# Kernel tuning notes

Measured on AMD Instinct MI355X. Metric: run time of the kernel, lower is better.

## Reference

```python
import jax, jax.numpy as jnp
import numpy as np

# Each of the 16 differentiable binary logic ops op_k(a,b) is a polynomial
# c0 + ca*a + cb*b + cab*(a*b). Rows follow the standard difflogic op table
# (op 3 = 'a' pass-through, matching the residual init in the source).
_OP2POLY = np.array([
    [0, 0, 0, 0],    # 0: False
    [0, 0, 0, 1],    # 1: a AND b
    [0, 1, 0, -1],   # 2: a AND NOT b
    [0, 1, 0, 0],    # 3: a
    [0, 0, 1, -1],   # 4: NOT a AND b
    [0, 0, 1, 0],    # 5: b
    [0, 1, 1, -2],   # 6: XOR
    [0, 1, 1, -1],   # 7: OR
    [1, -1, -1, 1],  # 8: NOR
    [1, -1, -1, 2],  # 9: XNOR
    [1, 0, -1, 0],   # 10: NOT b
    [1, 0, -1, 1],   # 11: a OR NOT b
    [1, -1, 0, 0],   # 12: NOT a
    [1, -1, 0, 1],   # 13: NOT a OR b
    [1, 0, 0, -1],   # 14: NAND
    [1, 0, 0, 0],    # 15: True
], dtype=np.float32)

KERNEL_SIZE, STRIDE, PADDING, GROUPS, TREE_DEPTH, TAU = 3, 1, 1, 1, 4, 1.0


def setup_inputs() -> dict:
    key = jax.random.key(0)
    k0, k1, k2, k3, k4 = jax.random.split(key, 5)
    B, Cin, H, W = 16, 64, 64, 64
    OC, N = 128, 2 ** TREE_DEPTH
    x = jax.random.uniform(k0, (B, Cin, H, W), dtype=jnp.float32)
    weights = jax.random.normal(k1, (OC, N - 1, 16), dtype=jnp.float32)
    ci = jax.random.randint(k2, (OC, N), 0, Cin // GROUPS, dtype=jnp.int32)
    px = jax.random.randint(k3, (OC, N), 0, KERNEL_SIZE, dtype=jnp.int32)
    py = jax.random.randint(k4, (OC, N), 0, KERNEL_SIZE, dtype=jnp.int32)
    return {"x": x, "weights": weights, "input_channel_indices": ci,
            "input_pos_x_indices": px, "input_pos_y_indices": py}


def _forward(x, weights, ci, px, py):
    B, Cin, H, W = x.shape
    OC = weights.shape[0]
    N = 2 ** TREE_DEPTH
    # Training-mode weights with straight-through estimator:
    # value = one_hot(argmax), gradient flows through softmax.
    w_soft = jax.nn.softmax(weights / TAU, axis=-1).astype(x.dtype)
    w_hard = jax.nn.one_hot(jnp.argmax(weights, axis=-1), 16, dtype=x.dtype)
    w = w_soft + jax.lax.stop_gradient(w_hard - w_soft)
    # [OC, num_gates, 4] polynomial coefficients over (1, a, b, ab)
    coeffs = jnp.einsum('ogk,kc->ogc', w, jnp.asarray(_OP2POLY, x.dtype))

    xp = jnp.pad(x, ((0, 0), (0, 0), (PADDING, PADDING), (PADDING, PADDING)))
    oh = (H + 2 * PADDING - KERNEL_SIZE) // STRIDE + 1
    ow = (W + 2 * PADDING - KERNEL_SIZE) // STRIDE + 1

    icpg = Cin // GROUPS
    group_of_oc = jnp.arange(OC, dtype=jnp.int32) // (OC // GROUPS)
    chan = group_of_oc[:, None] * icpg + ci                       # [OC, N]
    rows = (jnp.arange(oh, dtype=jnp.int32) * STRIDE)[None, None, :] + py[:, :, None]  # [OC,N,oh]
    cols = (jnp.arange(ow, dtype=jnp.int32) * STRIDE)[None, None, :] + px[:, :, None]  # [OC,N,ow]
    # Irregular per-output gather: [B, OC, N, oh, ow]
    vals = xp[:, chan[:, :, None, None], rows[:, :, :, None], cols[:, :, None, :]]

    # Binary tree of logic gates, level by level (gates stored leaf-level first).
    gate_off = 0
    for _ in range(TREE_DEPTH):
        n = vals.shape[2] // 2
        a, b = vals[:, :, 0::2], vals[:, :, 1::2]
        cc = coeffs[:, gate_off:gate_off + n]                     # [OC, n, 4]
        c0, ca, cb, cab = (cc[None, :, :, i, None, None] for i in range(4))
        vals = c0 + ca * a + cb * b + cab * (a * b)
        gate_off += n
    y = vals[:, :, 0]                                             # [B, OC, oh, ow]

    # 2x2 OR-pool (soft OR = 1 - prod(1 - v)), floor division of spatial dims.
    ph, pw = oh // 2, ow // 2
    y = y[:, :, :ph * 2, :pw * 2].reshape(B, OC, ph, 2, pw, 2)
    return 1.0 - jnp.prod(1.0 - y, axis=(3, 5))


def reference(x, weights, input_channel_indices, input_pos_x_indices, input_pos_y_indices):
    return _forward(x, weights, input_channel_indices, input_pos_x_indices, input_pos_y_indices)
```

## Files before the change

### kernel.cpp

```cpp
#include <hip/hip_runtime.h>

#define BATCH 16
#define CIN   64
#define H_    64
#define W_    64
#define IMG   (H_ * W_)
#define OCH   128
#define NLEAF 16
#define NGATE 15
#define PH    32
#define PW    32

__device__ __constant__ float OP2POLY[16][4] = {
    {0, 0, 0, 0}, {0, 0, 0, 1}, {0, 1, 0, -1}, {0, 1, 0, 0},
    {0, 0, 1, -1}, {0, 0, 1, 0}, {0, 1, 1, -2}, {0, 1, 1, -1},
    {1, -1, -1, 1}, {1, -1, -1, 2}, {1, 0, -1, 0}, {1, 0, -1, 1},
    {1, -1, 0, 0}, {1, -1, 0, 1}, {1, 0, 0, -1}, {1, 0, 0, 0}};

static __device__ __forceinline__ float readlane_f(float v, int l) {
    return __builtin_bit_cast(float,
        __builtin_amdgcn_readlane(__builtin_bit_cast(int, v), l));
}

__global__ __launch_bounds__(256, 4) void logic_tree_fused(
    const float* __restrict__ x,
    const float* __restrict__ weights,
    const int* __restrict__ ci,
    const int* __restrict__ px,
    const int* __restrict__ py,
    float* __restrict__ out)
{
    const int blk = blockIdx.x;
    const int xcd = blk & 7;
    const int jj  = blk >> 3;
    const int b   = (xcd << 1) | (jj >> 7);
    const int oc  = jj & 127;

    const int tid  = threadIdx.x;
    const int wave = tid >> 6;
    const int lane = tid & 63;
    const int row0 = wave << 4;

    const int g = (lane < NGATE) ? lane : 0;
    const float* wp = weights + (oc * NGATE + g) * 16;
    const float4 w0 = reinterpret_cast<const float4*>(wp)[0];
    const float4 w1 = reinterpret_cast<const float4*>(wp)[1];
    const float4 w2 = reinterpret_cast<const float4*>(wp)[2];
    const float4 w3 = reinterpret_cast<const float4*>(wp)[3];
    const float wv[16] = {w0.x, w0.y, w0.z, w0.w, w1.x, w1.y, w1.z, w1.w,
                          w2.x, w2.y, w2.z, w2.w, w3.x, w3.y, w3.z, w3.w};
    int best = 0;
    float bv = wv[0];
#pragma unroll
    for (int k = 1; k < 16; ++k)
        if (wv[k] > bv) { bv = wv[k]; best = k; }
    const float4 cf = reinterpret_cast<const float4*>(OP2POLY)[best];

    float C[NGATE * 4];
#pragma unroll
    for (int gg = 0; gg < NGATE; ++gg) {
        C[4 * gg + 0] = readlane_f(cf.x, gg);
        C[4 * gg + 1] = readlane_f(cf.y, gg);
        C[4 * gg + 2] = readlane_f(cf.z, gg);
        C[4 * gg + 3] = readlane_f(cf.w, gg);
    }

    int   voff[NLEAF];
    float fm[NLEAF];
    int   dyv[NLEAF];
#pragma unroll
    for (int n = 0; n < NLEAF; ++n) {
        const int ch = ci[oc * NLEAF + n];
        const int dy = py[oc * NLEAF + n] - 1;
        const int dx = px[oc * NLEAF + n] - 1;
        const int c  = lane + dx;
        const int ccl = min(max(c, 0), W_ - 1);
        voff[n] = ch * IMG + (row0 + dy) * W_ + ccl + W_;
        fm[n]   = ((unsigned)c < (unsigned)W_) ? 1.0f : 0.0f;
        dyv[n]  = dy;
    }
    const float* xb = x + ((size_t)b * CIN * IMG) - W_;

    float acc[NLEAF];
#pragma unroll
    for (int n = 0; n < NLEAF; ++n) {
        const bool bad = (row0 + dyv[n]) < 0;
        acc[n] = xb[voff[n] + (bad ? W_ : 0)] * (bad ? 0.0f : fm[n]);
    }

    const size_t obase =
        (((size_t)b * OCH + oc) * PH + (row0 >> 1)) * PW + (lane >> 1);

    float pprev = 0.0f;
#pragma unroll
    for (int k = 0; k < 16; ++k) {
        float nxt[NLEAF];
        if (k < 15) {
#pragma unroll
            for (int n = 0; n < NLEAF; ++n) {
                if (k == 14) {
                    const bool bad = (row0 + 15 + dyv[n]) > (H_ - 1);
                    nxt[n] = xb[voff[n] + 15 * W_ - (bad ? W_ : 0)] *
                             (bad ? 0.0f : 1.0f);
                } else {
                    nxt[n] = xb[voff[n] + (k + 1) * W_];
                }
            }
        }

        float v[NLEAF];
#pragma unroll
        for (int n = 0; n < NLEAF; ++n)
            v[n] = (k == 0) ? acc[n] : acc[n] * fm[n];

        int go = 0;
#pragma unroll
        for (int lev = 8; lev >= 1; lev >>= 1) {
#pragma unroll
            for (int t = 0; t < lev; ++t) {
                const float a  = v[2 * t];
                const float bb = v[2 * t + 1];
                v[t] = C[(go + t) * 4] + C[(go + t) * 4 + 1] * a +
                       C[(go + t) * 4 + 2] * bb + C[(go + t) * 4 + 3] * (a * bb);
            }
            go += lev;
        }

        const float q = 1.0f - v[0];
        if (k & 1) {
            const float p  = pprev * q;
            const float pp = p * __shfl_xor(p, 1, 64);
            if (!(lane & 1))
                out[obase + (size_t)(k >> 1) * PW] = 1.0f - pp;
        } else {
            pprev = q;
        }

        if (k < 15) {
#pragma unroll
            for (int n = 0; n < NLEAF; ++n) acc[n] = nxt[n];
        }
    }
}

extern "C" void kernel_launch(void* const* d_in, const int* in_sizes, int n_in,
                              void* d_out, int out_size, void* d_ws, size_t ws_size,
                              hipStream_t stream) {
    const float* x       = (const float*)d_in[0];
    const float* weights = (const float*)d_in[1];
    const int*   ci      = (const int*)d_in[2];
    const int*   px      = (const int*)d_in[3];
    const int*   py      = (const int*)d_in[4];
    float* out = (float*)d_out;
    (void)d_ws; (void)ws_size;

    logic_tree_fused<<<BATCH * OCH, 256, 0, stream>>>(x, weights, ci, px, py, out);
}
```

Measured before the change: 98.60 us.

## Stage input row strips in LDS and loop all output channels per block

Replaces the one-block-per-(batch, output channel) kernel with one block per (batch, 4-row strip). Each block loads all 64 channels of a 6-row haloed strip into shared memory once, and each wave then processes 8 output channels. Gather reads come from LDS instead of global/L2, and the argmax/op table and leaf indices are built once per block in shared memory. The trade-offs are a 1024-thread block with about 110KB of LDS, only 256 blocks, and redundant argmax work over all 1920 gates in every block.

After: 101.0 us. 2.4% more time.

```diff
diff --git a/kernel.cpp b/kernel.cpp
--- a/kernel.cpp
+++ b/kernel.cpp
@@ -11,18 +11,23 @@
 #define PH    32
 #define PW    32
 
-__device__ __constant__ float OP2POLY[16][4] = {
+#define XS_F   0
+#define LEAF_F 24576
+#define OPS_F  26624
+#define ZF     27136
+#define SMEM_F 27520
+
+__device__ __constant__ __align__(16) float OP2POLY[16][4] = {
     {0, 0, 0, 0}, {0, 0, 0, 1}, {0, 1, 0, -1}, {0, 1, 0, 0},
     {0, 0, 1, -1}, {0, 0, 1, 0}, {0, 1, 1, -2}, {0, 1, 1, -1},
     {1, -1, -1, 1}, {1, -1, -1, 2}, {1, 0, -1, 0}, {1, 0, -1, 1},
     {1, -1, 0, 0}, {1, -1, 0, 1}, {1, 0, 0, -1}, {1, 0, 0, 0}};
 
-static __device__ __forceinline__ float readlane_f(float v, int l) {
-    return __builtin_bit_cast(float,
-        __builtin_amdgcn_readlane(__builtin_bit_cast(int, v), l));
+static __device__ __forceinline__ int rfl_i(int v) {
+    return __builtin_amdgcn_readfirstlane(v);
 }
 
-__global__ __launch_bounds__(256, 4) void logic_tree_fused(
+__global__ __launch_bounds__(1024) void logic_tree_lds(
     const float* __restrict__ x,
     const float* __restrict__ weights,
     const int* __restrict__ ci,
@@ -30,115 +35,123 @@
     const int* __restrict__ py,
     float* __restrict__ out)
 {
-    const int blk = blockIdx.x;
-    const int xcd = blk & 7;
-    const int jj  = blk >> 3;
-    const int b   = (xcd << 1) | (jj >> 7);
-    const int oc  = jj & 127;
+    __shared__ float smem[SMEM_F];
+    int* smem_i = (int*)smem;
+    unsigned char* smem_b = (unsigned char*)smem;
 
-    const int tid  = threadIdx.x;
+    const int blk   = blockIdx.x;
+    const int b     = blk >> 4;
+    const int strip = blk & 15;
+    const int r0    = strip << 2;
+    const int tid   = threadIdx.x;
+
+    const float4* xb4 = reinterpret_cast<const float4*>(x + (size_t)b * (CIN * IMG));
+#pragma unroll
+    for (int i = 0; i < 6; ++i) {
+        int fidx = tid + i * 1024;
+        int ch   = fidx / 96;
+        int rem  = fidx - ch * 96;
+        int row  = rem >> 4;
+        int c4   = rem & 15;
+        int gr   = r0 - 1 + row;
+        float4 val = make_float4(0.f, 0.f, 0.f, 0.f);
+        if ((unsigned)gr < (unsigned)H_)
+            val = xb4[((ch << 6) | gr) * 16 + c4];
+        *reinterpret_cast<float4*>(&smem[ch * 384 + row * 64 + c4 * 4]) = val;
+    }
+
+    if (tid < 384) smem[ZF + tid] = 0.0f;
+
+    for (int t = tid; t < OCH * NGATE; t += 1024) {
+        const float* wp = weights + t * 16;
+        int best = 0;
+        float bv = wp[0];
+#pragma unroll
+        for (int k = 1; k < 16; ++k) {
+            float v = wp[k];
+            if (v > bv) { bv = v; best = k; }
+        }
+        int oc = t / 15, g = t - oc * 15;
+        smem_b[OPS_F * 4 + oc * 16 + g] = (unsigned char)best;
+        if (g == 14) smem_b[OPS_F * 4 + oc * 16 + 15] = 0;
+    }
+
+    for (int t = tid; t < OCH * NLEAF; t += 1024)
+        smem_i[LEAF_F + t] = (ci[t] << 4) | (py[t] << 2) | px[t];
+
+    __syncthreads();
+
     const int wave = tid >> 6;
     const int lane = tid & 63;
-    const int row0 = wave << 4;
 
-    const int g = (lane < NGATE) ? lane : 0;
-    const float* wp = weights + (oc * NGATE + g) * 16;
-    const float4 w0 = reinterpret_cast<const float4*>(wp)[0];
-    const float4 w1 = reinterpret_cast<const float4*>(wp)[1];
-    const float4 w2 = reinterpret_cast<const float4*>(wp)[2];
-    const float4 w3 = reinterpret_cast<const float4*>(wp)[3];
-    const float wv[16] = {w0.x, w0.y, w0.z, w0.w, w1.x, w1.y, w1.z, w1.w,
-                          w2.x, w2.y, w2.z, w2.w, w3.x, w3.y, w3.z, w3.w};
-    int best = 0;
-    float bv = wv[0];
+#pragma unroll 1
+    for (int q = 0; q < 8; ++q) {
+        const int oc = wave * 8 + q;
+
+        const uint4 opsv =
+            *reinterpret_cast<const uint4*>(&smem[OPS_F + oc * 4]);
+        const unsigned ou[4] = {
+            (unsigned)rfl_i((int)opsv.x), (unsigned)rfl_i((int)opsv.y),
+            (unsigned)rfl_i((int)opsv.z), (unsigned)rfl_i((int)opsv.w)};
+        float C[NGATE * 4];
 #pragma unroll
-    for (int k = 1; k < 16; ++k)
-        if (wv[k] > bv) { bv = wv[k]; best = k; }
-    const float4 cf = reinterpret_cast<const float4*>(OP2POLY)[best];
-
-    float C[NGATE * 4];
-#pragma unroll
-    for (int gg = 0; gg < NGATE; ++gg) {
-        C[4 * gg + 0] = readlane_f(cf.x, gg);
-        C[4 * gg + 1] = readlane_f(cf.y, gg);
-        C[4 * gg + 2] = readlane_f(cf.z, gg);
-        C[4 * gg + 3] = readlane_f(cf.w, gg);
-    }
-
-    int   voff[NLEAF];
-    float fm[NLEAF];
-    int   dyv[NLEAF];
-#pragma unroll
-    for (int n = 0; n < NLEAF; ++n) {
-        const int ch = ci[oc * NLEAF + n];
-        const int dy = py[oc * NLEAF + n] - 1;
-        const int dx = px[oc * NLEAF + n] - 1;
-        const int c  = lane + dx;
-        const int ccl = min(max(c, 0), W_ - 1);
-        voff[n] = ch * IMG + (row0 + dy) * W_ + ccl + W_;
-        fm[n]   = ((unsigned)c < (unsigned)W_) ? 1.0f : 0.0f;
-        dyv[n]  = dy;
-    }
-    const float* xb = x + ((size_t)b * CIN * IMG) - W_;
-
-    float acc[NLEAF];
-#pragma unroll
-    for (int n = 0; n < NLEAF; ++n) {
-        const bool bad = (row0 + dyv[n]) < 0;
-        acc[n] = xb[voff[n] + (bad ? W_ : 0)] * (bad ? 0.0f : fm[n]);
-    }
-
-    const size_t obase =
-        (((size_t)b * OCH + oc) * PH + (row0 >> 1)) * PW + (lane >> 1);
-
-    float pprev = 0.0f;
-#pragma unroll
-    for (int k = 0; k < 16; ++k) {
-        float nxt[NLEAF];
-        if (k < 15) {
-#pragma unroll
-            for (int n = 0; n < NLEAF; ++n) {
-                if (k == 14) {
-                    const bool bad = (row0 + 15 + dyv[n]) > (H_ - 1);
-                    nxt[n] = xb[voff[n] + 15 * W_ - (bad ? W_ : 0)] *
-                             (bad ? 0.0f : 1.0f);
-                } else {
-                    nxt[n] = xb[voff[n] + (k + 1) * W_];
-                }
-            }
+        for (int g = 0; g < NGATE; ++g) {
+            int op = (ou[g >> 2] >> ((g & 3) * 8)) & 255;
+            const float4 cf = reinterpret_cast<const float4*>(OP2POLY)[op];
+            C[4 * g + 0] = cf.x;
+            C[4 * g + 1] = cf.y;
+            C[4 * g + 2] = cf.z;
+            C[4 * g + 3] = cf.w;
         }
 
-        float v[NLEAF];
+        int base[NLEAF];
 #pragma unroll
-        for (int n = 0; n < NLEAF; ++n)
-            v[n] = (k == 0) ? acc[n] : acc[n] * fm[n];
-
-        int go = 0;
-#pragma unroll
-        for (int lev = 8; lev >= 1; lev >>= 1) {
-#pragma unroll
-            for (int t = 0; t < lev; ++t) {
-                const float a  = v[2 * t];
-                const float bb = v[2 * t + 1];
-                v[t] = C[(go + t) * 4] + C[(go + t) * 4 + 1] * a +
-                       C[(go + t) * 4 + 2] * bb + C[(go + t) * 4 + 3] * (a * bb);
-            }
-            go += lev;
+        for (int n = 0; n < NLEAF; ++n) {
+            int pk = rfl_i(smem_i[LEAF_F + oc * 16 + n]);
+            int ch = pk >> 4;
+            int dy = ((pk >> 2) & 3) - 1;
+            int dx = (pk & 3) - 1;
+            int c  = lane + dx;
+            int ccl = min(max(c, 0), W_ - 1);
+            int bin = ch * 384 + (1 + dy) * 64 + ccl;
+            int bz  = ZF + (1 + dy) * 64 + lane;
+            base[n] = ((unsigned)c < (unsigned)W_) ? bin : bz;
         }
 
-        const float q = 1.0f - v[0];
-        if (k & 1) {
-            const float p  = pprev * q;
-            const float pp = p * __shfl_xor(p, 1, 64);
-            if (!(lane & 1))
-                out[obase + (size_t)(k >> 1) * PW] = 1.0f - pp;
-        } else {
-            pprev = q;
-        }
+        const size_t obase =
+            (((size_t)b * OCH + oc) * PH + (r0 >> 1)) * PW + (lane >> 1);
 
-        if (k < 15) {
+        float pprev = 0.0f;
 #pragma unroll
-            for (int n = 0; n < NLEAF; ++n) acc[n] = nxt[n];
+        for (int r = 0; r < 4; ++r) {
+            float v[NLEAF];
+#pragma unroll
+            for (int n = 0; n < NLEAF; ++n)
+                v[n] = smem[base[n] + r * 64];
+
+            int go = 0;
+#pragma unroll
+            for (int lev = 8; lev >= 1; lev >>= 1) {
+#pragma unroll
+                for (int t = 0; t < lev; ++t) {
+                    float a  = v[2 * t];
+                    float bb = v[2 * t + 1];
+                    v[t] = C[(go + t) * 4] + C[(go + t) * 4 + 1] * a +
+                           C[(go + t) * 4 + 2] * bb +
+                           C[(go + t) * 4 + 3] * (a * bb);
+                }
+                go += lev;
+            }
+
+            float qv = 1.0f - v[0];
+            if (r & 1) {
+                float p  = pprev * qv;
+                float pp = p * __shfl_xor(p, 1, 64);
+                if (!(lane & 1))
+                    out[obase + (size_t)(r >> 1) * PW] = 1.0f - pp;
+            } else {
+                pprev = qv;
+            }
         }
     }
 }
@@ -154,5 +167,5 @@
     float* out = (float*)d_out;
     (void)d_ws; (void)ws_size;
 
-    logic_tree_fused<<<BATCH * OCH, 256, 0, stream>>>(x, weights, ci, px, py, out);
+    logic_tree_lds<<<BATCH * 16, 1024, 0, stream>>>(x, weights, ci, px, py, out);
 }
```
